# Performance work log

Measured on AMD Instinct MI355X. Metric: run time of the kernel, lower is better.

## Reference

```python
import jax, jax.numpy as jnp
import numpy as np

DIM_HEAD = 128
HEADS = 16
SCALE = DIM_HEAD ** -0.5


def rotate_half(t):
    # '... (j d) -> ... j d' with j=2: split into first/second halves
    x1, x2 = jnp.split(t, 2, axis=-1)
    return jnp.concatenate((-x2, x1), axis=-1)


def apply_rope(pos, t):
    # pos: [n, d]; t: [..., n, d]
    return t * jnp.cos(pos) + rotate_half(t) * jnp.sin(pos)


def setup_inputs() -> dict:
    key = jax.random.key(0)
    k0, k1, k2, k3 = jax.random.split(key, 4)
    b, n, dim = 2, 2048, 2048
    inner = HEADS * DIM_HEAD
    return {
        "x": jax.random.normal(k0, (b, n, dim), jnp.float32),
        "Wq": jax.random.normal(k1, (dim, inner), jnp.float32) * 0.02,
        "Wkv": jax.random.normal(k2, (dim, 2 * DIM_HEAD), jnp.float32) * 0.02,
        "Wout": jax.random.normal(k3, (inner, dim), jnp.float32) * 0.02,
    }


def reference(x, Wq, Wkv, Wout):
    b, n, dim = x.shape
    # projections from the UN-normalized x (norm in original is dead code)
    q = x @ Wq                               # [b, n, h*d]
    kv = x @ Wkv                             # [b, n, 2d]
    k, v = jnp.split(kv, 2, axis=-1)         # each [b, n, d] (multi-query)
    q = q.reshape(b, n, HEADS, DIM_HEAD).transpose(0, 2, 1, 3)  # [b,h,n,d]

    # rotary positions
    inv_freq = 1.0 / (10000.0 ** (jnp.arange(0, DIM_HEAD, 2, dtype=jnp.float32) / DIM_HEAD))
    freqs = jnp.arange(n, dtype=jnp.float32)[:, None] * inv_freq[None, :]
    pos = jnp.concatenate((freqs, freqs), axis=-1)  # [n, d]

    q = apply_rope(pos, q) * SCALE
    k = apply_rope(pos, k)

    sim = jnp.einsum('bhid,bjd->bhij', q, k)  # [b,h,n,n]
    causal_mask = jnp.triu(jnp.ones((n, n), dtype=bool), 1)
    neg = -jnp.finfo(sim.dtype).max
    sim = jnp.where(causal_mask, neg, sim)
    sim = sim - jax.lax.stop_gradient(jnp.max(sim, axis=-1, keepdims=True))
    attn = jax.nn.softmax(sim, axis=-1)

    out = jnp.einsum('bhij,bjd->bhid', attn, v)          # [b,h,n,d]
    out = out.transpose(0, 2, 1, 3).reshape(b, n, HEADS * DIM_HEAD)
    return out @ Wout
```

## Files before the change

### kernel.cpp

```cpp
#include <hip/hip_runtime.h>
#include <hip/hip_bf16.h>
#include <cstddef>
#include <cstdint>

#define BATCH 2
#define SEQ   2048
#define DIM   2048
#define HEADS 16
#define DHEAD 128
#define INNER (HEADS * DHEAD)
#define MROWS (BATCH * SEQ)
#define ATT_SCALE 0.08838834764831845f
#define QK_SCALE (0.08838834764831845f * 1.4426950408889634f)
#define NEG_LOG2_10000_DIV64 (-13.287712379549449f / 64.0f)
#define M_HAT 12.0f

typedef __attribute__((ext_vector_type(8))) short short8;
typedef __attribute__((ext_vector_type(4))) short short4v;
typedef __attribute__((ext_vector_type(4))) float f32x4;

static __device__ __forceinline__ short f2bf(float x) {
    uint32_t u = __float_as_uint(x);
    uint32_t r = (u + 0x7fffu + ((u >> 16) & 1u)) >> 16;
    return (short)r;
}
static __device__ __forceinline__ float bf2f(short s) {
    return __uint_as_float(((uint32_t)(uint16_t)s) << 16);
}
static __device__ __forceinline__ short2 f2bf2(float a, float b) {
    __hip_bfloat162 h = __float22bfloat162_rn(make_float2(a, b));
    return *reinterpret_cast<short2*>(&h);
}

static __device__ __forceinline__ void glds16(const short* g, short* l) {
    __builtin_amdgcn_global_load_lds(
        (const __attribute__((address_space(1))) unsigned int*)g,
        (__attribute__((address_space(3))) unsigned int*)l, 16, 0, 0);
}

static __device__ __forceinline__ int swz_row(int r) {
    return (r & 3) | ((r >> 1) & 4);
}

static __device__ __forceinline__ void tcast_body(const float* __restrict__ W,
                                                  short* __restrict__ Wt,
                                                  int R, int C, int bx, int by,
                                                  int tid, float (*tile)[65]) {
    const int c0 = bx * 64, r0 = by * 64;
#pragma unroll
    for (int t = 0; t < 16; ++t) {
        int idx = tid + t * 256;
        int row = idx >> 6, col = idx & 63;
        tile[row][col] = W[(size_t)(r0 + row) * C + c0 + col];
    }
    __syncthreads();
#pragma unroll
    for (int t = 0; t < 16; ++t) {
        int idx = tid + t * 256;
        int r = idx >> 6, c = idx & 63;
        Wt[(size_t)(c0 + r) * R + r0 + c] = f2bf(tile[c][r]);
    }
}

__global__ __launch_bounds__(256) void prep(const float* __restrict__ x,
                                            short* __restrict__ xb,
                                            const float* __restrict__ Wq,
                                            short* __restrict__ Wt,
                                            const float* __restrict__ Wkv,
                                            short* __restrict__ Wkvt,
                                            const float* __restrict__ Wout,
                                            short* __restrict__ WtO,
                                            float2* __restrict__ lut) {
    __shared__ float tile[64][65];
    const int bid = blockIdx.x;
    const int tid = threadIdx.x;
    if (bid < 8192) {
        int i = bid * 256 + tid;
        float4 v = ((const float4*)x)[i];
        short2 s01 = f2bf2(v.x, v.y), s23 = f2bf2(v.z, v.w);
        short4v s = {s01.x, s01.y, s23.x, s23.y};
        ((short4v*)xb)[i] = s;
    } else if (bid < 9216) {
        int t = bid - 8192;
        tcast_body(Wq, Wt, DIM, INNER, t & 31, t >> 5, tid, tile);
    } else if (bid < 9344) {
        int t = bid - 9216;
        tcast_body(Wkv, Wkvt, DIM, 256, t & 3, t >> 2, tid, tile);
    } else if (bid < 10368) {
        int t = bid - 9344;
        tcast_body(Wout, WtO, INNER, DIM, t & 31, t >> 5, tid, tile);
    } else {
        int t = (bid - 10368) * 256 + tid;
        int pos = t >> 6, j = t & 63;
        float ang = (float)pos * exp2f((float)j * NEG_LOG2_10000_DIV64);
        lut[t] = make_float2(cosf(ang), sinf(ang));
    }
}

__global__ __launch_bounds__(256) void gemm_qkv(const short* __restrict__ A,
                                                const short* __restrict__ Bt,
                                                short* __restrict__ qout,
                                                short* __restrict__ kvout) {
    __shared__ __align__(16) short sA[128 * 32];
    __shared__ __align__(16) short sB[128 * 32];
    const int K = DIM;

    const int tid = threadIdx.x;
    const int w = tid >> 6, lane = tid & 63;
    const int ln = lane & 15, qr = lane >> 4;
    const int bm = blockIdx.y * 128, bn = blockIdx.x * 128;
    const int wm = (w >> 1) * 64, wn = (w & 1) * 64;

    const f32x4 zero4 = {0.f, 0.f, 0.f, 0.f};
    f32x4 acc[4][4];
#pragma unroll
    for (int mt = 0; mt < 4; ++mt)
#pragma unroll
        for (int nt = 0; nt < 4; ++nt) acc[mt][nt] = zero4;

    const int srow = lane >> 2;
    const short* pA = A + (size_t)(bm + w * 32 + srow) * K + (lane & 3) * 8;
    const short* pB = Bt + (size_t)(bn + w * 32 + srow) * K + (lane & 3) * 8;
    short* lA = &sA[(w * 32) * 32];
    short* lB = &sB[(w * 32) * 32];

    for (int k0 = 0; k0 < K; k0 += 32) {
        __syncthreads();
        glds16(pA + k0, lA);
        glds16(pA + k0 + (size_t)16 * K, lA + 512);
        glds16(pB + k0, lB);
        glds16(pB + k0 + (size_t)16 * K, lB + 512);
        __syncthreads();

        short8 af[4], bfr[4];
#pragma unroll
        for (int mt = 0; mt < 4; ++mt)
            af[mt] = *(const short8*)&sA[(wm + mt * 16 + ln) * 32 + qr * 8];
#pragma unroll
        for (int nt = 0; nt < 4; ++nt)
            bfr[nt] = *(const short8*)&sB[(wn + nt * 16 + ln) * 32 + qr * 8];
#pragma unroll
        for (int mt = 0; mt < 4; ++mt)
#pragma unroll
            for (int nt = 0; nt < 4; ++nt)
                acc[mt][nt] = __builtin_amdgcn_mfma_f32_16x16x32_bf16(
                    af[mt], bfr[nt], acc[mt][nt], 0, 0, 0);
    }

    short* C;
    int stride, colb;
    if (bn < INNER) { C = qout; stride = INNER; colb = bn; }
    else            { C = kvout; stride = 256;  colb = bn - INNER; }
#pragma unroll
    for (int mt = 0; mt < 4; ++mt)
#pragma unroll
        for (int nt = 0; nt < 4; ++nt)
#pragma unroll
            for (int r = 0; r < 4; ++r)
                C[(size_t)(bm + wm + mt * 16 + qr * 4 + r) * stride +
                  colb + wn + nt * 16 + ln] = f2bf(acc[mt][nt][r]);
}

__global__ __launch_bounds__(256) void gemm_bt(const short* __restrict__ A,
                                               const short* __restrict__ Bt,
                                               float* __restrict__ C,
                                               int M, int N, int K) {
    __shared__ __align__(16) short sA[128 * 32];
    __shared__ __align__(16) short sB[128 * 32];

    const int tid = threadIdx.x;
    const int w = tid >> 6, lane = tid & 63;
    const int ln = lane & 15, qr = lane >> 4;
    const int bm = blockIdx.y * 128, bn = blockIdx.x * 128;
    const int wm = (w >> 1) * 64, wn = (w & 1) * 64;

    const f32x4 zero4 = {0.f, 0.f, 0.f, 0.f};
    f32x4 acc[4][4];
#pragma unroll
    for (int mt = 0; mt < 4; ++mt)
#pragma unroll
        for (int nt = 0; nt < 4; ++nt) acc[mt][nt] = zero4;

    const int srow = lane >> 2;
    const short* pA = A + (size_t)(bm + w * 32 + srow) * K + (lane & 3) * 8;
    const short* pB = Bt + (size_t)(bn + w * 32 + srow) * K + (lane & 3) * 8;
    short* lA = &sA[(w * 32) * 32];
    short* lB = &sB[(w * 32) * 32];

    for (int k0 = 0; k0 < K; k0 += 32) {
        __syncthreads();
        glds16(pA + k0, lA);
        glds16(pA + k0 + (size_t)16 * K, lA + 512);
        glds16(pB + k0, lB);
        glds16(pB + k0 + (size_t)16 * K, lB + 512);
        __syncthreads();

        short8 af[4], bfr[4];
#pragma unroll
        for (int mt = 0; mt < 4; ++mt)
            af[mt] = *(const short8*)&sA[(wm + mt * 16 + ln) * 32 + qr * 8];
#pragma unroll
        for (int nt = 0; nt < 4; ++nt)
            bfr[nt] = *(const short8*)&sB[(wn + nt * 16 + ln) * 32 + qr * 8];
#pragma unroll
        for (int mt = 0; mt < 4; ++mt)
#pragma unroll
            for (int nt = 0; nt < 4; ++nt)
                acc[mt][nt] = __builtin_amdgcn_mfma_f32_16x16x32_bf16(
                    af[mt], bfr[nt], acc[mt][nt], 0, 0, 0);
    }

#pragma unroll
    for (int mt = 0; mt < 4; ++mt)
#pragma unroll
        for (int nt = 0; nt < 4; ++nt)
#pragma unroll
            for (int r = 0; r < 4; ++r)
                C[(size_t)(bm + wm + mt * 16 + qr * 4 + r) * N +
                  bn + wn + nt * 16 + ln] = acc[mt][nt][r];
}

__global__ __launch_bounds__(256) void rope_q_v(short* __restrict__ qb,
                                                const float2* __restrict__ lut) {
    int idx = blockIdx.x * 256 + threadIdx.x;
    int c = idx & 7;
    int rh = idx >> 3;
    int pos = (rh >> 4) & (SEQ - 1);
    short* row = qb + ((size_t)rh << 7);
    short8 a8 = *(short8*)&row[c * 8];
    short8 b8 = *(short8*)&row[64 + c * 8];
    const float2* lp = &lut[pos * 64 + c * 8];
    short8 o1, o2;
#pragma unroll
    for (int e = 0; e < 8; e += 2) {
        float2 cs0 = lp[e], cs1 = lp[e + 1];
        float a0 = bf2f(a8[e]), b0 = bf2f(b8[e]);
        float a1 = bf2f(a8[e + 1]), b1 = bf2f(b8[e + 1]);
        short2 p1 = f2bf2((a0 * cs0.x - b0 * cs0.y) * QK_SCALE,
                          (a1 * cs1.x - b1 * cs1.y) * QK_SCALE);
        short2 p2 = f2bf2((b0 * cs0.x + a0 * cs0.y) * QK_SCALE,
                          (b1 * cs1.x + a1 * cs1.y) * QK_SCALE);
        o1[e] = p1.x; o1[e + 1] = p1.y;
        o2[e] = p2.x; o2[e + 1] = p2.y;
    }
    *(short8*)&row[c * 8] = o1;
    *(short8*)&row[64 + c * 8] = o2;
}

__global__ __launch_bounds__(256) void prep_kv(const short* __restrict__ kvbb,
                                               short* __restrict__ kb,
                                               short* __restrict__ vt,
                                               const float2* __restrict__ lut) {
    __shared__ float tile[64][65];
    const int bid = blockIdx.x;
    const int tid = threadIdx.x;
    if (bid < 128) {
        const int b = bid >> 6;
        const int tile_id = bid & 63;
        const int p0 = (tile_id >> 1) * 64;
        const int d0 = (tile_id & 1) * 64;
#pragma unroll
        for (int t = 0; t < 16; ++t) {
            int idx = tid + t * 256;
            int row = idx >> 6, col = idx & 63;
            tile[row][col] = bf2f(kvbb[((size_t)(b * SEQ) + p0 + row) * 256 + 128 + d0 + col]);
        }
        __syncthreads();
#pragma unroll
        for (int t = 0; t < 16; ++t) {
            int idx = tid + t * 256;
            int r = idx >> 6, c = idx & 63;
            vt[((size_t)(b * DHEAD) + d0 + r) * SEQ + p0 + c] = f2bf(tile[c][r]);
        }
    } else {
        int t = (bid - 128) * 256 + tid;
        int c = t & 7;
        int bn = t >> 3;
        int pos = bn & (SEQ - 1);
        const short* row = kvbb + (size_t)bn * 256;
        short* orow = kb + ((size_t)bn << 7);
        short8 a8 = *(const short8*)&row[c * 8];
        short8 b8 = *(const short8*)&row[64 + c * 8];
        const float2* lp = &lut[pos * 64 + c * 8];
        short8 o1, o2;
#pragma unroll
        for (int e = 0; e < 8; e += 2) {
            float2 cs0 = lp[e], cs1 = lp[e + 1];
            float a0 = bf2f(a8[e]), b0 = bf2f(b8[e]);
            float a1 = bf2f(a8[e + 1]), b1 = bf2f(b8[e + 1]);
            short2 p1 = f2bf2(a0 * cs0.x - b0 * cs0.y, a1 * cs1.x - b1 * cs1.y);
            short2 p2 = f2bf2(b0 * cs0.x + a0 * cs0.y, b1 * cs1.x + a1 * cs1.y);
            o1[e] = p1.x; o1[e + 1] = p1.y;
            o2[e] = p2.x; o2[e + 1] = p2.y;
        }
        *(short8*)&orow[c * 8] = o1;
        *(short8*)&orow[64 + c * 8] = o2;
    }
}

__global__ __launch_bounds__(512) void attn_mfma(const short* __restrict__ qb,
                                                 const short* __restrict__ kb,
                                                 const short* __restrict__ vt,
                                                 short* __restrict__ o) {
    __shared__ __align__(16) short sK[2][2][64 * 128];
    __shared__ __align__(16) short sV[2][2][128 * 64];
    __shared__ float lred[4][2][64];

    const int bid = blockIdx.x;
    const int p = bid & 7;
    const int bh = bid >> 3;
    const int h = bh & (HEADS - 1);
    const int b = bh >> 4;

    const int tid = threadIdx.x;
    const int w = tid >> 6;
    const int g = w >> 2;
    const int wg = w & 3;
    const int lane = tid & 63;
    const int ln = lane & 15;
    const int qr = lane >> 4;

    const short* kbase = kb + (size_t)b * SEQ * DHEAD;
    const short* vbase = vt + (size_t)b * DHEAD * SEQ;

    int offK[4], offV[4], ldsK[4], ldsV[4];
#pragma unroll
    for (int t = 0; t < 4; ++t) {
        int rk = wg * 16 + t * 4 + (lane >> 4);
        int ck = (lane & 15) ^ swz_row(rk);
        offK[t] = rk * DHEAD + ck * 8;
        ldsK[t] = (wg * 16 + t * 4) * 128;
        int rv = wg * 32 + t * 8 + (lane >> 3);
        int cv = (lane & 7) ^ swz_row(rv);
        offV[t] = rv * SEQ + cv * 8;
        ldsV[t] = (wg * 32 + t * 8) * 64;
    }

    for (int ph = 0; ph < 2; ++ph) {
        const int it = ph ? p : (15 - p);
        const int i0 = it * 128;
        const int njt = 2 * it + 2;
        const int half = njt >> 1;

        short8 qf[2][4];
#pragma unroll
        for (int qs = 0; qs < 2; ++qs) {
            const size_t qrow =
                ((size_t)(b * SEQ + i0 + wg * 32 + qs * 16 + ln)) * INNER + h * DHEAD;
#pragma unroll
            for (int ks = 0; ks < 4; ++ks)
                qf[qs][ks] = *(const short8*)&qb[qrow + ks * 32 + qr * 8];
        }

        const f32x4 zero4 = {0.f, 0.f, 0.f, 0.f};
        f32x4 oa[2][8];
#pragma unroll
        for (int qs = 0; qs < 2; ++qs)
#pragma unroll
            for (int dt = 0; dt < 8; ++dt) oa[qs][dt] = zero4;
        float lsum[2] = {0.f, 0.f};

        __syncthreads();
        {
            const size_t kof = (size_t)g * 64 * DHEAD;
            const size_t vof = (size_t)g * 64;
#pragma unroll
            for (int t = 0; t < 4; ++t)
                glds16(kbase + kof + offK[t], &sK[g][0][ldsK[t]]);
#pragma unroll
            for (int t = 0; t < 4; ++t)
                glds16(vbase + vof + offV[t], &sV[g][0][ldsV[t]]);
        }

        for (int k = 0; k < half; ++k) {
            const int cur = k & 1;
            const int jt = 2 * k + g;
            __syncthreads();
            if (k + 1 < half) {
                const size_t kof = (size_t)(jt + 2) * 64 * DHEAD;
                const size_t vof = (size_t)(jt + 2) * 64;
#pragma unroll
                for (int t = 0; t < 4; ++t)
                    glds16(kbase + kof + offK[t], &sK[g][cur ^ 1][ldsK[t]]);
#pragma unroll
                for (int t = 0; t < 4; ++t)
                    glds16(vbase + vof + offV[t], &sV[g][cur ^ 1][ldsV[t]]);
            }

            f32x4 sacc[2][4];
#pragma unroll
            for (int qs = 0; qs < 2; ++qs)
#pragma unroll
                for (int nt = 0; nt < 4; ++nt) sacc[qs][nt] = zero4;
#pragma unroll
            for (int nt = 0; nt < 4; ++nt) {
                const int row = ((nt >> 1) << 5) + ((ln >> 2) << 3) +
                                ((nt & 1) << 2) + (ln & 3);
                const int sw = ln & 7;
#pragma unroll
                for (int ks = 0; ks < 4; ++ks) {
                    short8 kf = *(const short8*)&sK[g][cur][row * 128 + ((4 * ks + qr) ^ sw) * 8];
                    sacc[0][nt] = __builtin_amdgcn_mfma_f32_16x16x32_bf16(
                        kf, qf[0][ks], sacc[0][nt], 0, 0, 0);
                    sacc[1][nt] = __builtin_amdgcn_mfma_f32_16x16x32_bf16(
                        kf, qf[1][ks], sacc[1][nt], 0, 0, 0);
                }
            }

            short8 pb[2][2];
#pragma unroll
            for (int qs = 0; qs < 2; ++qs) {
                const int ig = i0 + wg * 32 + qs * 16 + ln;
                if (jt * 64 + 63 > ig) {
#pragma unroll
                    for (int nt = 0; nt < 4; ++nt)
#pragma unroll
                        for (int r = 0; r < 4; ++r) {
                            int jg = jt * 64 + ((nt >> 1) << 5) + qr * 8 +
                                     ((nt & 1) << 2) + r;
                            if (jg > ig) sacc[qs][nt][r] = -3.0e38f;
                        }
                }
                float rs = 0.f;
                float pv[4][4];
#pragma unroll
                for (int nt = 0; nt < 4; ++nt)
#pragma unroll
                    for (int r = 0; r < 4; ++r) {
                        float e = exp2f(sacc[qs][nt][r] - M_HAT);
                        pv[nt][r] = e;
                        rs += e;
                    }
                rs += __shfl_xor(rs, 16);
                rs += __shfl_xor(rs, 32);
                lsum[qs] += rs;
#pragma unroll
                for (int kb2 = 0; kb2 < 2; ++kb2) {
                    short2* pp = (short2*)&pb[qs][kb2];
                    pp[0] = f2bf2(pv[2 * kb2][0], pv[2 * kb2][1]);
                    pp[1] = f2bf2(pv[2 * kb2][2], pv[2 * kb2][3]);
                    pp[2] = f2bf2(pv[2 * kb2 + 1][0], pv[2 * kb2 + 1][1]);
                    pp[3] = f2bf2(pv[2 * kb2 + 1][2], pv[2 * kb2 + 1][3]);
                }
            }

#pragma unroll
            for (int kb2 = 0; kb2 < 2; ++kb2) {
#pragma unroll
                for (int dt = 0; dt < 8; ++dt) {
                    const int row = dt * 16 + ln;
                    short8 vf = *(const short8*)&sV[g][cur][row * 64 +
                        ((4 * kb2 + qr) ^ swz_row(row)) * 8];
                    oa[0][dt] = __builtin_amdgcn_mfma_f32_16x16x32_bf16(
                        vf, pb[0][kb2], oa[0][dt], 0, 0, 0);
                    oa[1][dt] = __builtin_amdgcn_mfma_f32_16x16x32_bf16(
                        vf, pb[1][kb2], oa[1][dt], 0, 0, 0);
                }
            }
        }

        f32x4* cb = (f32x4*)&sK[1][0][0];
        __syncthreads();
        if (g == 1) {
#pragma unroll
            for (int dt = 0; dt < 8; ++dt)
                cb[dt * 256 + wg * 64 + lane] = oa[0][dt];
            lred[wg][0][lane] = lsum[0];
            lred[wg][1][lane] = lsum[1];
        }
        __syncthreads();
        if (g == 0) {
#pragma unroll
            for (int dt = 0; dt < 8; ++dt)
                oa[0][dt] += cb[dt * 256 + wg * 64 + lane];
            lsum[0] += lred[wg][0][lane];
            lsum[1] += lred[wg][1][lane];
        }
        __syncthreads();
        if (g == 1) {
#pragma unroll
            for (int dt = 0; dt < 8; ++dt)
                cb[dt * 256 + wg * 64 + lane] = oa[1][dt];
        }
        __syncthreads();
        if (g == 0) {
#pragma unroll
            for (int dt = 0; dt < 8; ++dt)
                oa[1][dt] += cb[dt * 256 + wg * 64 + lane];
#pragma unroll
            for (int qs = 0; qs < 2; ++qs) {
                const float invl = 1.f / lsum[qs];
                short* orow = o + ((size_t)(b * SEQ + i0 + wg * 32 + qs * 16 + ln)) * INNER +
                              h * DHEAD;
#pragma unroll
                for (int dt = 0; dt < 8; ++dt) {
                    short2 s01 = f2bf2(oa[qs][dt][0] * invl, oa[qs][dt][1] * invl);
                    short2 s23 = f2bf2(oa[qs][dt][2] * invl, oa[qs][dt][3] * invl);
                    short4v sv = {s01.x, s01.y, s23.x, s23.y};
                    *(short4v*)&orow[dt * 16 + qr * 4] = sv;
                }
            }
        }
    }
}

extern "C" void kernel_launch(void* const* d_in, const int* in_sizes, int n_in,
                              void* d_out, int out_size, void* d_ws, size_t ws_size,
                              hipStream_t stream) {
    const float* x    = (const float*)d_in[0];
    const float* Wq   = (const float*)d_in[1];
    const float* Wkv  = (const float*)d_in[2];
    const float* Wout = (const float*)d_in[3];
    float* out = (float*)d_out;

    short* xb    = (short*)d_ws;
    short* Wt    = xb + (size_t)MROWS * DIM;
    short* Wkvt  = Wt + (size_t)DIM * INNER;
    short* WtO   = Wkvt + (size_t)256 * DIM;
    short* qb    = WtO + (size_t)DIM * INNER;
    short* kvbb  = qb + (size_t)MROWS * INNER;
    short* kb    = kvbb + (size_t)MROWS * 256;
    short* vt    = kb + (size_t)MROWS * DHEAD;
    float2* lut  = (float2*)(vt + (size_t)BATCH * DHEAD * SEQ);
    short* ob    = xb;

    prep<<<10880, 256, 0, stream>>>(x, xb, Wq, Wt, Wkv, Wkvt, Wout, WtO, lut);
    gemm_qkv<<<dim3(18, 32), 256, 0, stream>>>(xb, Wt, qb, kvbb);
    rope_q_v<<<(MROWS * HEADS * 8) / 256, 256, 0, stream>>>(qb, lut);
    prep_kv<<<256, 256, 0, stream>>>(kvbb, kb, vt, lut);
    attn_mfma<<<256, 512, 0, stream>>>(qb, kb, vt, ob);
    gemm_bt<<<dim3(DIM / 128, MROWS / 128), 256, 0, stream>>>(ob, WtO, out, MROWS, DIM, INNER);
}
```

Baseline: 289.2 us.

## Merge rope kernels, truncate P to bf16, interleave PV MFMAs, halve reduction syncs

```diff
diff --git a/kernel.cpp b/kernel.cpp
--- a/kernel.cpp
+++ b/kernel.cpp
@@ -28,8 +28,11 @@
     return __uint_as_float(((uint32_t)(uint16_t)s) << 16);
 }
 static __device__ __forceinline__ short2 f2bf2(float a, float b) {
-    __hip_bfloat162 h = __float22bfloat162_rn(make_float2(a, b));
-    return *reinterpret_cast<short2*>(&h);
+    short2 r; r.x = f2bf(a); r.y = f2bf(b); return r;
+}
+static __device__ __forceinline__ uint32_t pk_trunc(float p0, float p1) {
+    return __builtin_amdgcn_perm(__float_as_uint(p1), __float_as_uint(p0),
+                                 0x07060302u);
 }
 
 static __device__ __forceinline__ void glds16(const short* g, short* l) {
@@ -220,43 +223,42 @@
                   bn + wn + nt * 16 + ln] = acc[mt][nt][r];
 }
 
-__global__ __launch_bounds__(256) void rope_q_v(short* __restrict__ qb,
+__global__ __launch_bounds__(256) void rope_all(short* __restrict__ qb,
+                                                const short* __restrict__ kvbb,
+                                                short* __restrict__ kb,
+                                                short* __restrict__ vt,
                                                 const float2* __restrict__ lut) {
-    int idx = blockIdx.x * 256 + threadIdx.x;
-    int c = idx & 7;
-    int rh = idx >> 3;
-    int pos = (rh >> 4) & (SEQ - 1);
-    short* row = qb + ((size_t)rh << 7);
-    short8 a8 = *(short8*)&row[c * 8];
-    short8 b8 = *(short8*)&row[64 + c * 8];
-    const float2* lp = &lut[pos * 64 + c * 8];
-    short8 o1, o2;
-#pragma unroll
-    for (int e = 0; e < 8; e += 2) {
-        float2 cs0 = lp[e], cs1 = lp[e + 1];
-        float a0 = bf2f(a8[e]), b0 = bf2f(b8[e]);
-        float a1 = bf2f(a8[e + 1]), b1 = bf2f(b8[e + 1]);
-        short2 p1 = f2bf2((a0 * cs0.x - b0 * cs0.y) * QK_SCALE,
-                          (a1 * cs1.x - b1 * cs1.y) * QK_SCALE);
-        short2 p2 = f2bf2((b0 * cs0.x + a0 * cs0.y) * QK_SCALE,
-                          (b1 * cs1.x + a1 * cs1.y) * QK_SCALE);
-        o1[e] = p1.x; o1[e + 1] = p1.y;
-        o2[e] = p2.x; o2[e + 1] = p2.y;
-    }
-    *(short8*)&row[c * 8] = o1;
-    *(short8*)&row[64 + c * 8] = o2;
-}
-
-__global__ __launch_bounds__(256) void prep_kv(const short* __restrict__ kvbb,
-                                               short* __restrict__ kb,
-                                               short* __restrict__ vt,
-                                               const float2* __restrict__ lut) {
     __shared__ float tile[64][65];
     const int bid = blockIdx.x;
     const int tid = threadIdx.x;
-    if (bid < 128) {
-        const int b = bid >> 6;
-        const int tile_id = bid & 63;
+    if (bid < 2048) {
+        int idx = bid * 256 + tid;
+        int c = idx & 7;
+        int rh = idx >> 3;
+        int pos = (rh >> 4) & (SEQ - 1);
+        short* row = qb + ((size_t)rh << 7);
+        short8 a8 = *(short8*)&row[c * 8];
+        short8 b8 = *(short8*)&row[64 + c * 8];
+        const float2* lp = &lut[pos * 64 + c * 8];
+        short8 o1, o2;
+#pragma unroll
+        for (int e = 0; e < 8; e += 2) {
+            float2 cs0 = lp[e], cs1 = lp[e + 1];
+            float a0 = bf2f(a8[e]), b0 = bf2f(b8[e]);
+            float a1 = bf2f(a8[e + 1]), b1 = bf2f(b8[e + 1]);
+            short2 p1 = f2bf2((a0 * cs0.x - b0 * cs0.y) * QK_SCALE,
+                              (a1 * cs1.x - b1 * cs1.y) * QK_SCALE);
+            short2 p2 = f2bf2((b0 * cs0.x + a0 * cs0.y) * QK_SCALE,
+                              (b1 * cs1.x + a1 * cs1.y) * QK_SCALE);
+            o1[e] = p1.x; o1[e + 1] = p1.y;
+            o2[e] = p2.x; o2[e + 1] = p2.y;
+        }
+        *(short8*)&row[c * 8] = o1;
+        *(short8*)&row[64 + c * 8] = o2;
+    } else if (bid < 2176) {
+        const int t0 = bid - 2048;
+        const int b = t0 >> 6;
+        const int tile_id = t0 & 63;
         const int p0 = (tile_id >> 1) * 64;
         const int d0 = (tile_id & 1) * 64;
 #pragma unroll
@@ -273,7 +275,7 @@
             vt[((size_t)(b * DHEAD) + d0 + r) * SEQ + p0 + c] = f2bf(tile[c][r]);
         }
     } else {
-        int t = (bid - 128) * 256 + tid;
+        int t = (bid - 2176) * 256 + tid;
         int c = t & 7;
         int bn = t >> 3;
         int pos = bn & (SEQ - 1);
@@ -407,6 +409,7 @@
                 }
             }
 
+            short8 vfc[2][8];
             short8 pb[2][2];
 #pragma unroll
             for (int qs = 0; qs < 2; ++qs) {
@@ -436,57 +439,50 @@
                 lsum[qs] += rs;
 #pragma unroll
                 for (int kb2 = 0; kb2 < 2; ++kb2) {
-                    short2* pp = (short2*)&pb[qs][kb2];
-                    pp[0] = f2bf2(pv[2 * kb2][0], pv[2 * kb2][1]);
-                    pp[1] = f2bf2(pv[2 * kb2][2], pv[2 * kb2][3]);
-                    pp[2] = f2bf2(pv[2 * kb2 + 1][0], pv[2 * kb2 + 1][1]);
-                    pp[3] = f2bf2(pv[2 * kb2 + 1][2], pv[2 * kb2 + 1][3]);
+                    uint32_t* pp = (uint32_t*)&pb[qs][kb2];
+                    pp[0] = pk_trunc(pv[2 * kb2][0], pv[2 * kb2][1]);
+                    pp[1] = pk_trunc(pv[2 * kb2][2], pv[2 * kb2][3]);
+                    pp[2] = pk_trunc(pv[2 * kb2 + 1][0], pv[2 * kb2 + 1][1]);
+                    pp[3] = pk_trunc(pv[2 * kb2 + 1][2], pv[2 * kb2 + 1][3]);
+                }
+
+#pragma unroll
+                for (int kb2 = 0; kb2 < 2; ++kb2) {
+#pragma unroll
+                    for (int dt = 0; dt < 8; ++dt) {
+                        if (qs == 0) {
+                            const int row = dt * 16 + ln;
+                            vfc[kb2][dt] = *(const short8*)&sV[g][cur][row * 64 +
+                                ((4 * kb2 + qr) ^ swz_row(row)) * 8];
+                        }
+                        oa[qs][dt] = __builtin_amdgcn_mfma_f32_16x16x32_bf16(
+                            vfc[kb2][dt], pb[qs][kb2], oa[qs][dt], 0, 0, 0);
+                    }
                 }
             }
-
-#pragma unroll
-            for (int kb2 = 0; kb2 < 2; ++kb2) {
-#pragma unroll
-                for (int dt = 0; dt < 8; ++dt) {
-                    const int row = dt * 16 + ln;
-                    short8 vf = *(const short8*)&sV[g][cur][row * 64 +
-                        ((4 * kb2 + qr) ^ swz_row(row)) * 8];
-                    oa[0][dt] = __builtin_amdgcn_mfma_f32_16x16x32_bf16(
-                        vf, pb[0][kb2], oa[0][dt], 0, 0, 0);
-                    oa[1][dt] = __builtin_amdgcn_mfma_f32_16x16x32_bf16(
-                        vf, pb[1][kb2], oa[1][dt], 0, 0, 0);
-                }
+        }
+
+        f32x4* cb0 = (f32x4*)&sK[1][0][0];
+        f32x4* cb1 = (f32x4*)&sV[1][0][0];
+        __syncthreads();
+        if (g == 1) {
+#pragma unroll
+            for (int dt = 0; dt < 8; ++dt) {
+                cb0[dt * 256 + wg * 64 + lane] = oa[0][dt];
+                cb1[dt * 256 + wg * 64 + lane] = oa[1][dt];
             }
-        }
-
-        f32x4* cb = (f32x4*)&sK[1][0][0];
-        __syncthreads();
-        if (g == 1) {
-#pragma unroll
-            for (int dt = 0; dt < 8; ++dt)
-                cb[dt * 256 + wg * 64 + lane] = oa[0][dt];
             lred[wg][0][lane] = lsum[0];
             lred[wg][1][lane] = lsum[1];
         }
         __syncthreads();
         if (g == 0) {
-#pragma unroll
-            for (int dt = 0; dt < 8; ++dt)
-                oa[0][dt] += cb[dt * 256 + wg * 64 + lane];
             lsum[0] += lred[wg][0][lane];
             lsum[1] += lred[wg][1][lane];
-        }
-        __syncthreads();
-        if (g == 1) {
-#pragma unroll
-            for (int dt = 0; dt < 8; ++dt)
-                cb[dt * 256 + wg * 64 + lane] = oa[1][dt];
-        }
-        __syncthreads();
-        if (g == 0) {
-#pragma unroll
-            for (int dt = 0; dt < 8; ++dt)
-                oa[1][dt] += cb[dt * 256 + wg * 64 + lane];
+#pragma unroll
+            for (int dt = 0; dt < 8; ++dt) {
+                oa[0][dt] += cb0[dt * 256 + wg * 64 + lane];
+                oa[1][dt] += cb1[dt * 256 + wg * 64 + lane];
+            }
 #pragma unroll
             for (int qs = 0; qs < 2; ++qs) {
                 const float invl = 1.f / lsum[qs];
@@ -526,8 +522,7 @@
 
     prep<<<10880, 256, 0, stream>>>(x, xb, Wq, Wt, Wkv, Wkvt, Wout, WtO, lut);
     gemm_qkv<<<dim3(18, 32), 256, 0, stream>>>(xb, Wt, qb, kvbb);
-    rope_q_v<<<(MROWS * HEADS * 8) / 256, 256, 0, stream>>>(qb, lut);
-    prep_kv<<<256, 256, 0, stream>>>(kvbb, kb, vt, lut);
+    rope_all<<<2304, 256, 0, stream>>>(qb, kvbb, kb, vt, lut);
     attn_mfma<<<256, 512, 0, stream>>>(qb, kb, vt, ob);
     gemm_bt<<<dim3(DIM / 128, MROWS / 128), 256, 0, stream>>>(ob, WtO, out, MROWS, DIM, INNER);
 }
```

New measurement: 299.2 us. +3.5%, slower.
